# Kernel tuning notes

Hardware: AMD Instinct MI355X
Metric: run time of the kernel (lower is better)

## Reference

```python
import jax, jax.numpy as jnp
import numpy as np

N = 10000   # nodes
E = 160000  # edges (avg degree 16)
IN = 512
HID = 512
OUT = 512


def setup_inputs() -> dict:
    key = jax.random.key(0)
    ks = jax.random.split(key, 8)
    x = jax.random.normal(ks[0], (N, IN), dtype=jnp.float32)
    edge_index = jax.random.randint(ks[1], (2, E), 0, N, dtype=jnp.int64)
    def w(k, fi, fo):
        return jax.random.normal(k, (fi, fo), dtype=jnp.float32) * (1.0 / np.sqrt(fi)).astype(np.float32)
    return {
        "x": x,
        "edge_index": edge_index,
        "W1": w(ks[2], IN, HID), "b1": jnp.zeros((HID,), jnp.float32),
        "W2": w(ks[3], HID, HID), "b2": jnp.zeros((HID,), jnp.float32),
        "W3": w(ks[4], HID, OUT), "b3": jnp.zeros((OUT,), jnp.float32),
    }


def _gcn_norm(edge_index, n):
    # add self loops, then symmetric normalization D^{-1/2} (A+I) D^{-1/2}
    loops = jnp.arange(n, dtype=edge_index.dtype)
    row = jnp.concatenate([edge_index[0], loops])  # source
    col = jnp.concatenate([edge_index[1], loops])  # target (aggregation dim)
    deg = jax.ops.segment_sum(jnp.ones_like(col, jnp.float32), col, num_segments=n)
    dis = jnp.where(deg > 0, jax.lax.rsqrt(jnp.maximum(deg, 1.0)), 0.0)
    norm = dis[row] * dis[col]  # [E+N]
    return row, col, norm


def _gcn_layer(x, row, col, norm, W, b, n):
    h = x @ W                                    # [N, d_out] dense GEMM
    msg = h[row] * norm[:, None]                 # gather + scale, [E+N, d_out]
    out = jax.ops.segment_sum(msg, col, num_segments=n)  # scatter-add
    return out + b


def reference(x, edge_index, W1, b1, W2, b2, W3, b3):
    n = x.shape[0]
    row, col, norm = _gcn_norm(edge_index, n)
    h = _gcn_layer(x, row, col, norm, W1, b1, n)
    h = jax.nn.relu(h)  # dropout is identity in eval mode
    h = _gcn_layer(h, row, col, norm, W2, b2, n)
    h = jax.nn.relu(h)
    h = _gcn_layer(h, row, col, norm, W3, b3, n)
    return h
```

## Files before the change

kernel.cpp:

```cpp
#include <hip/hip_runtime.h>

typedef __attribute__((ext_vector_type(8))) short bf16x8;
typedef __attribute__((ext_vector_type(4))) float f32x4;

#define N_NODES 10000
#define N_EDGES 160000
#define FDIM    512
#define ELL     64
#define BM 64
#define BN 128
#define BK 64
#define TM 157
#define NGEMM (TM * 4)
#define NSCAT 625
#define NTRAN 768
#define NZERO 40
#define FBM 48
#define FNB 209
#define APAD 520

__device__ __forceinline__ float bf2f(unsigned int u) {
    union { unsigned int i; float f; } v; v.i = u << 16; return v.f;
}
__device__ __forceinline__ float bfs2f(short s) {
    return bf2f((unsigned int)(unsigned short)s);
}
__device__ __forceinline__ unsigned short f2bf(float f) {
    union { float f; unsigned int u; } v; v.f = f;
    unsigned int u = v.u;
    unsigned int r = u + 0x7fffu + ((u >> 16) & 1u);
    return (unsigned short)(r >> 16);
}
__device__ __forceinline__ void gload_lds16(const void* g, void* l) {
    __builtin_amdgcn_global_load_lds(
        (const __attribute__((address_space(1))) unsigned int*)g,
        (__attribute__((address_space(3))) unsigned int*)l, 16, 0, 0);
}
__device__ __forceinline__ int wave_is_f32(const unsigned int* w) {
    unsigned int v = w[(size_t)(threadIdx.x & 63) * 1000];
    unsigned int ex = (v >> 7) & 0xFFu;
    unsigned long long inb = __ballot(ex >= 100u && ex <= 140u);
    return (__popcll(inb) >= 48) ? 0 : 1;
}

__global__ __launch_bounds__(256) void prep_v8(
        const void* __restrict__ x, const void* __restrict__ ei,
        const void* __restrict__ W1, const void* __restrict__ W2,
        const void* __restrict__ W3, unsigned short* __restrict__ Wt,
        int* __restrict__ cnt, int* __restrict__ flags) {
    int b = blockIdx.x, tid = threadIdx.x;
    if (b < NTRAN) {
        __shared__ unsigned short tile[32][33];
        int z = b >> 8, t = b & 255;
        const void* W = (z == 0) ? W1 : (z == 1) ? W2 : W3;
        unsigned short* outp = Wt + (size_t)z * FDIM * FDIM;
        int ff32 = wave_is_f32((const unsigned int*)W);
        int tx = tid & 31, ty = tid >> 5;
        int xcol = (t & 15) * 32 + tx;
        int y0 = (t >> 4) * 32 + ty;
        #pragma unroll
        for (int j = 0; j < 32; j += 8) {
            int idx = (y0 + j) * FDIM + xcol;
            tile[ty + j][tx] = ff32 ? f2bf(((const float*)W)[idx])
                                    : ((const unsigned short*)W)[idx];
        }
        __syncthreads();
        int x2 = (t >> 4) * 32 + tx;
        int y2 = (t & 15) * 32 + ty;
        #pragma unroll
        for (int j = 0; j < 32; j += 8)
            outp[(y2 + j) * FDIM + x2] = tile[tx][ty + j];
    } else if (b < NTRAN + NZERO) {
        int i = (b - NTRAN) * 256 + tid;
        if (i < N_NODES) cnt[i] = 0;
    } else {
        if (tid < 64) {
            const unsigned long long* e64 = (const unsigned long long*)ei;
            unsigned long long v = e64[(size_t)tid * 2500];
            unsigned long long big = __ballot(v > 0xFFFFFFFFull);
            const unsigned int* xw = (const unsigned int*)x;
            unsigned int w = xw[(size_t)tid * 1000];
            unsigned int ex = (w >> 7) & 0xFFu;
            unsigned long long inb = __ballot(ex >= 100u && ex <= 140u);
            if (tid == 0) {
                flags[0] = (big == 0ull) ? 1 : 0;
                flags[1] = (__popcll(inb) >= 48) ? 0 : 1;
            }
        }
    }
}

__global__ __launch_bounds__(256) void gemm_scat_v8(
        const void* __restrict__ Ap, const unsigned short* __restrict__ Bt,
        unsigned short* __restrict__ C, const int* __restrict__ flags,
        const void* __restrict__ ei, int* __restrict__ cnt,
        int* __restrict__ ell) {
    __shared__ unsigned short As[BM * BK];
    __shared__ unsigned short Bs[BN * BK];
    if (blockIdx.x >= NGEMM) {
        int e = (blockIdx.x - NGEMM) * 256 + threadIdx.x;
        if (e < N_EDGES) {
            int r, c;
            if (flags[0]) {
                r = (int)((const long long*)ei)[e];
                c = (int)((const long long*)ei)[N_EDGES + e];
            } else {
                r = ((const int*)ei)[e];
                c = ((const int*)ei)[N_EDGES + e];
            }
            int slot = atomicAdd(&cnt[c], 1);
            if (slot < ELL) ell[(size_t)c * ELL + slot] = r;
        }
        return;
    }
    const int K = FDIM;
    const int af32 = flags[1];
    const int tid = threadIdx.x;
    const int t = blockIdx.x;
    const int bm = (t % TM) * BM, bn = (t / TM) * BN;
    const int lane = tid & 63, wv = tid >> 6;
    const int wm = (wv >> 1) * 32, wn = (wv & 1) * 64;
    const int lrow = lane & 15;
    const int tsl = lane >> 4;
    const int ksw = (lane & 7) ^ ((lane >> 3) & 7);
    const unsigned short* Abf = (const unsigned short*)Ap;
    f32x4 acc[2][4] = {};

    for (int k0 = 0; k0 < K; k0 += BK) {
        if (!af32) {
            #pragma unroll
            for (int j = 0; j < 2; ++j) {
                int r0 = wv * 16 + j * 8;
                int arow = bm + r0 + (lane >> 3);
                if (arow >= N_NODES) arow = N_NODES - 1;
                gload_lds16(Abf + (size_t)arow * K + k0 + ksw * 8, &As[r0 * BK]);
            }
            #pragma unroll
            for (int j = 0; j < 4; ++j) {
                int r0 = wv * 32 + j * 8;
                gload_lds16(Bt + (size_t)(bn + r0 + (lane >> 3)) * K + k0 + ksw * 8,
                            &Bs[r0 * BK]);
            }
        } else {
            #pragma unroll
            for (int j = 0; j < 4; ++j) {
                int r0 = wv * 32 + j * 8;
                gload_lds16(Bt + (size_t)(bn + r0 + (lane >> 3)) * K + k0 + ksw * 8,
                            &Bs[r0 * BK]);
            }
            #pragma unroll
            for (int i = 0; i < 2; ++i) {
                int c = tid + i * 256;
                int row = c >> 3, sl = c & 7;
                int grow = bm + row;
                bf16x8 va = {};
                if (grow < N_NODES) {
                    const float* Af = (const float*)Ap + (size_t)grow * K + k0 + sl * 8;
                    f32x4 lo = *(const f32x4*)Af;
                    f32x4 hi = *(const f32x4*)(Af + 4);
                    #pragma unroll
                    for (int jj = 0; jj < 4; ++jj) {
                        va[jj]     = (short)f2bf(lo[jj]);
                        va[4 + jj] = (short)f2bf(hi[jj]);
                    }
                }
                *(bf16x8*)(&As[row * BK + ((sl ^ (row & 7)) * 8)]) = va;
            }
        }
        __syncthreads();
        #pragma unroll
        for (int half = 0; half < 2; ++half) {
            int ts = half * 4 + tsl;
            bf16x8 af[2], bfr[4];
            #pragma unroll
            for (int f = 0; f < 2; ++f) {
                int row = wm + f * 16 + lrow;
                af[f] = *(const bf16x8*)(&As[row * BK + ((ts ^ (lrow & 7)) * 8)]);
            }
            #pragma unroll
            for (int f = 0; f < 4; ++f) {
                int row = wn + f * 16 + lrow;
                bfr[f] = *(const bf16x8*)(&Bs[row * BK + ((ts ^ (lrow & 7)) * 8)]);
            }
            #pragma unroll
            for (int fm = 0; fm < 2; ++fm)
                #pragma unroll
                for (int fn = 0; fn < 4; ++fn)
                    acc[fm][fn] = __builtin_amdgcn_mfma_f32_16x16x32_bf16(
                        af[fm], bfr[fn], acc[fm][fn], 0, 0, 0);
        }
        __syncthreads();
    }

    int crow = (lane >> 4) * 4;
    int ccol = lane & 15;
    #pragma unroll
    for (int fm = 0; fm < 2; ++fm)
        #pragma unroll
        for (int fn = 0; fn < 4; ++fn)
            #pragma unroll
            for (int r = 0; r < 4; ++r) {
                int row = bm + wm + fm * 16 + crow + r;
                if (row < N_NODES)
                    C[(size_t)row * FDIM + bn + wn + fn * 16 + ccol] =
                        f2bf(acc[fm][fn][r]);
            }
}

__global__ __launch_bounds__(384) void fused_ag_v8(
        const unsigned short* __restrict__ gin, const void* __restrict__ bias,
        const int* __restrict__ cnt, const int* __restrict__ ell,
        const unsigned short* __restrict__ Bt, unsigned short* __restrict__ Cout,
        const int* __restrict__ flags) {
    __shared__ unsigned short As[FBM * APAD];
    __shared__ unsigned short Bs[512 * 64];
    const int tid = threadIdx.x, lane = tid & 63, wv = tid / 64;
    const int bm = blockIdx.x * FBM;
    const int ff32 = flags[1];
    const int ksw = (lane & 7) ^ ((lane >> 3) & 7);

    for (int m = wv; m < 64; m += 6) {
        int r0 = m * 8;
        gload_lds16(Bt + (size_t)(r0 + (lane >> 3)) * FDIM + 0 + ksw * 8,
                    &Bs[r0 * 64]);
    }

    for (int rl = wv * 8; rl < wv * 8 + 8; ++rl) {
        int i = bm + rl;
        float a[8] = {};
        if (i < N_NODES) {
            int ci = cnt[i];
            int re = (ci > ELL) ? ELL : ci;
            const int* ep = ell + (size_t)i * ELL;
            int   srcl = (lane < re) ? ep[lane] : 0;
            int   cl   = (lane < re) ? cnt[srcl] : 0;
            float wl = rsqrtf((float)(cl + 1) * (float)(ci + 1));
            int j = 0;
            for (; j + 8 <= re; j += 8) {
                int s[8]; float w[8]; bf16x8 v[8];
                #pragma unroll
                for (int q = 0; q < 8; ++q) {
                    s[q] = __shfl(srcl, j + q); w[q] = __shfl(wl, j + q);
                }
                #pragma unroll
                for (int q = 0; q < 8; ++q)
                    v[q] = *(const bf16x8*)(gin + (size_t)s[q] * FDIM + lane * 8);
                #pragma unroll
                for (int q = 0; q < 8; ++q)
                    #pragma unroll
                    for (int tt = 0; tt < 8; ++tt) a[tt] += w[q] * bfs2f(v[q][tt]);
            }
            for (; j < re; ++j) {
                int s = __shfl(srcl, j); float w = __shfl(wl, j);
                bf16x8 v = *(const bf16x8*)(gin + (size_t)s * FDIM + lane * 8);
                #pragma unroll
                for (int tt = 0; tt < 8; ++tt) a[tt] += w * bfs2f(v[tt]);
            }
            float wself = 1.0f / (float)(ci + 1);
            bf16x8 vs = *(const bf16x8*)(gin + (size_t)i * FDIM + lane * 8);
            #pragma unroll
            for (int tt = 0; tt < 8; ++tt) a[tt] += wself * bfs2f(vs[tt]);
            if (ff32) {
                const float* B = (const float*)bias + lane * 8;
                #pragma unroll
                for (int tt = 0; tt < 8; ++tt) a[tt] += B[tt];
            } else {
                bf16x8 bb = *(const bf16x8*)((const unsigned short*)bias + lane * 8);
                #pragma unroll
                for (int tt = 0; tt < 8; ++tt) a[tt] += bfs2f(bb[tt]);
            }
            #pragma unroll
            for (int tt = 0; tt < 8; ++tt) a[tt] = fmaxf(a[tt], 0.f);
        }
        bf16x8 o;
        #pragma unroll
        for (int tt = 0; tt < 8; ++tt) o[tt] = (short)f2bf(a[tt]);
        *(bf16x8*)(&As[rl * APAD + lane * 8]) = o;
    }
    __syncthreads();

    const int wrow = wv % 3, wcol = wv / 3;
    const int lrow = lane & 15, tsl = lane >> 4;
    f32x4 acc[16] = {};
    for (int k0 = 0; k0 < FDIM; k0 += 64) {
        #pragma unroll
        for (int half = 0; half < 2; ++half) {
            bf16x8 af = *(const bf16x8*)(
                &As[(wrow * 16 + lrow) * APAD + k0 + half * 32 + tsl * 8]);
            int ts = half * 4 + tsl;
            #pragma unroll
            for (int ct = 0; ct < 16; ++ct) {
                int n = wcol * 256 + ct * 16 + lrow;
                bf16x8 bfr = *(const bf16x8*)(
                    &Bs[n * 64 + ((ts ^ (lrow & 7)) * 8)]);
                acc[ct] = __builtin_amdgcn_mfma_f32_16x16x32_bf16(
                    af, bfr, acc[ct], 0, 0, 0);
            }
        }
        __syncthreads();
        if (k0 + 64 < FDIM) {
            for (int m = wv; m < 64; m += 6) {
                int r0 = m * 8;
                gload_lds16(Bt + (size_t)(r0 + (lane >> 3)) * FDIM + (k0 + 64) + ksw * 8,
                            &Bs[r0 * 64]);
            }
        }
        __syncthreads();
    }
    int crow = (lane >> 4) * 4, ccol = lane & 15;
    #pragma unroll
    for (int ct = 0; ct < 16; ++ct)
        #pragma unroll
        for (int r = 0; r < 4; ++r) {
            int grow = bm + wrow * 16 + crow + r;
            if (grow < N_NODES)
                Cout[(size_t)grow * FDIM + wcol * 256 + ct * 16 + ccol] =
                    f2bf(acc[ct][r]);
        }
}

__global__ __launch_bounds__(256) void agg3_v8(
        const unsigned short* __restrict__ g, const void* __restrict__ bias,
        const int* __restrict__ cnt, const int* __restrict__ ell,
        void* __restrict__ out, const int* __restrict__ flags) {
    int wv = threadIdx.x >> 6, lane = threadIdx.x & 63;
    int i = blockIdx.x * 2 + (wv >> 1);
    int f = (wv & 1) * 256 + lane * 4;
    int ci = cnt[i];
    int re = (ci > ELL) ? ELL : ci;
    const int* ep = ell + (size_t)i * ELL;
    int   srcl = (lane < re) ? ep[lane] : 0;
    int   cl   = (lane < re) ? cnt[srcl] : 0;
    float wl = rsqrtf((float)(cl + 1) * (float)(ci + 1));
    float a0 = 0.f, a1 = 0.f, a2 = 0.f, a3 = 0.f;
    int j = 0;
    for (; j + 4 <= re; j += 4) {
        int s0 = __shfl(srcl, j);     float w0 = __shfl(wl, j);
        int s1 = __shfl(srcl, j + 1); float w1 = __shfl(wl, j + 1);
        int s2 = __shfl(srcl, j + 2); float w2 = __shfl(wl, j + 2);
        int s3 = __shfl(srcl, j + 3); float w3 = __shfl(wl, j + 3);
        uint2 v0 = *(const uint2*)(g + (size_t)s0 * FDIM + f);
        uint2 v1 = *(const uint2*)(g + (size_t)s1 * FDIM + f);
        uint2 v2 = *(const uint2*)(g + (size_t)s2 * FDIM + f);
        uint2 v3 = *(const uint2*)(g + (size_t)s3 * FDIM + f);
        a0 += w0 * bf2f(v0.x & 0xffffu); a1 += w0 * bf2f(v0.x >> 16);
        a2 += w0 * bf2f(v0.y & 0xffffu); a3 += w0 * bf2f(v0.y >> 16);
        a0 += w1 * bf2f(v1.x & 0xffffu); a1 += w1 * bf2f(v1.x >> 16);
        a2 += w1 * bf2f(v1.y & 0xffffu); a3 += w1 * bf2f(v1.y >> 16);
        a0 += w2 * bf2f(v2.x & 0xffffu); a1 += w2 * bf2f(v2.x >> 16);
        a2 += w2 * bf2f(v2.y & 0xffffu); a3 += w2 * bf2f(v2.y >> 16);
        a0 += w3 * bf2f(v3.x & 0xffffu); a1 += w3 * bf2f(v3.x >> 16);
        a2 += w3 * bf2f(v3.y & 0xffffu); a3 += w3 * bf2f(v3.y >> 16);
    }
    for (; j < re; ++j) {
        int s = __shfl(srcl, j); float w = __shfl(wl, j);
        uint2 v = *(const uint2*)(g + (size_t)s * FDIM + f);
        a0 += w * bf2f(v.x & 0xffffu); a1 += w * bf2f(v.x >> 16);
        a2 += w * bf2f(v.y & 0xffffu); a3 += w * bf2f(v.y >> 16);
    }
    float wself = 1.0f / (float)(ci + 1);
    uint2 vs = *(const uint2*)(g + (size_t)i * FDIM + f);
    a0 += wself * bf2f(vs.x & 0xffffu); a1 += wself * bf2f(vs.x >> 16);
    a2 += wself * bf2f(vs.y & 0xffffu); a3 += wself * bf2f(vs.y >> 16);
    int ff32 = flags[1];
    if (ff32) {
        f32x4 bb = *(const f32x4*)((const float*)bias + f);
        a0 += bb[0]; a1 += bb[1]; a2 += bb[2]; a3 += bb[3];
        f32x4 o = {a0, a1, a2, a3};
        *(f32x4*)((float*)out + (size_t)i * FDIM + f) = o;
    } else {
        uint2 bb = *(const uint2*)((const unsigned short*)bias + f);
        a0 += bf2f(bb.x & 0xffffu); a1 += bf2f(bb.x >> 16);
        a2 += bf2f(bb.y & 0xffffu); a3 += bf2f(bb.y >> 16);
        uint2 o;
        o.x = (unsigned int)f2bf(a0) | ((unsigned int)f2bf(a1) << 16);
        o.y = (unsigned int)f2bf(a2) | ((unsigned int)f2bf(a3) << 16);
        *(uint2*)((unsigned short*)out + (size_t)i * FDIM + f) = o;
    }
}

extern "C" void kernel_launch(void* const* d_in, const int* in_sizes, int n_in,
                              void* d_out, int out_size, void* d_ws, size_t ws_size,
                              hipStream_t stream) {
    (void)in_sizes; (void)n_in; (void)out_size; (void)ws_size;
    const void* x  = d_in[0];
    const void* ei = d_in[1];
    const void* W1 = d_in[2];
    const void* b1 = d_in[3];
    const void* W2 = d_in[4];
    const void* b2 = d_in[5];
    const void* W3 = d_in[6];
    const void* b3 = d_in[7];

    char* p = (char*)d_ws;
    auto alloc = [&](size_t bytes) -> void* {
        void* r = (void*)p;
        p += (bytes + 255) & ~(size_t)255;
        return r;
    };
    int*  flags = (int*) alloc(16);
    int*  cnt   = (int*) alloc((size_t)N_NODES * 4);
    int*  ell   = (int*) alloc((size_t)N_NODES * ELL * 4);
    unsigned short* Wt = (unsigned short*)alloc((size_t)3 * FDIM * FDIM * 2);
    unsigned short* g  = (unsigned short*)alloc((size_t)N_NODES * FDIM * 2);

    unsigned short* Wt1 = Wt;
    unsigned short* Wt2 = Wt + (size_t)FDIM * FDIM;
    unsigned short* Wt3 = Wt + (size_t)2 * FDIM * FDIM;
    unsigned short* h   = (unsigned short*)d_out;

    prep_v8<<<NTRAN + NZERO + 1, 256, 0, stream>>>(x, ei, W1, W2, W3, Wt, cnt, flags);
    gemm_scat_v8<<<NGEMM + NSCAT, 256, 0, stream>>>(x, Wt1, g, flags, ei, cnt, ell);
    fused_ag_v8<<<FNB, 384, 0, stream>>>(g, b1, cnt, ell, Wt2, h, flags);
    fused_ag_v8<<<FNB, 384, 0, stream>>>(h, b2, cnt, ell, Wt3, g, flags);
    agg3_v8<<<N_NODES / 2, 256, 0, stream>>>(g, b3, cnt, ell, d_out, flags);
}
```

Measured before the change: 228.6 us.

## Unfuse aggregation from GEMM and slice aggregation by feature columns

Replaces the fused aggregate-then-GEMM kernel, which used only 209 large blocks, with separate launches: a standalone GEMM per layer and a feature-sliced aggregation kernel. The aggregation splits the 512 features into 4 slices of 128 and launches one wave per node per slice, with 8-way unrolled gathers. The aim is more parallelism and better cache locality for the gathers, since each slice's working set is smaller. In exchange it adds extra kernel launches and an intermediate round trip through global memory for h.

```diff
diff --git a/kernel.cpp b/kernel.cpp
--- a/kernel.cpp
+++ b/kernel.cpp
@@ -15,15 +15,12 @@
 #define NSCAT 625
 #define NTRAN 768
 #define NZERO 40
-#define FBM 48
-#define FNB 209
-#define APAD 520
+#define SLICES 4
+#define SLW 128
+#define SLB 2500
 
 __device__ __forceinline__ float bf2f(unsigned int u) {
     union { unsigned int i; float f; } v; v.i = u << 16; return v.f;
-}
-__device__ __forceinline__ float bfs2f(short s) {
-    return bf2f((unsigned int)(unsigned short)s);
 }
 __device__ __forceinline__ unsigned short f2bf(float f) {
     union { float f; unsigned int u; } v; v.f = f;
@@ -43,7 +40,7 @@
     return (__popcll(inb) >= 48) ? 0 : 1;
 }
 
-__global__ __launch_bounds__(256) void prep_v8(
+__global__ __launch_bounds__(256) void prep_v9(
         const void* __restrict__ x, const void* __restrict__ ei,
         const void* __restrict__ W1, const void* __restrict__ W2,
         const void* __restrict__ W3, unsigned short* __restrict__ Wt,
@@ -90,11 +87,11 @@
     }
 }
 
-__global__ __launch_bounds__(256) void gemm_scat_v8(
+__global__ __launch_bounds__(256) void gemm_v9(
         const void* __restrict__ Ap, const unsigned short* __restrict__ Bt,
-        unsigned short* __restrict__ C, const int* __restrict__ flags,
-        const void* __restrict__ ei, int* __restrict__ cnt,
-        int* __restrict__ ell) {
+        unsigned short* __restrict__ C, int a_ext,
+        const int* __restrict__ flags, const void* __restrict__ ei,
+        int* __restrict__ cnt, int* __restrict__ ell) {
     __shared__ unsigned short As[BM * BK];
     __shared__ unsigned short Bs[BN * BK];
     if (blockIdx.x >= NGEMM) {
@@ -114,7 +111,7 @@
         return;
     }
     const int K = FDIM;
-    const int af32 = flags[1];
+    const int af32 = a_ext ? flags[1] : 0;
     const int tid = threadIdx.x;
     const int t = blockIdx.x;
     const int bm = (t % TM) * BM, bn = (t / TM) * BN;
@@ -207,175 +204,73 @@
             }
 }
 
-__global__ __launch_bounds__(384) void fused_ag_v8(
+__global__ __launch_bounds__(256) void agg_sl_v9(
         const unsigned short* __restrict__ gin, const void* __restrict__ bias,
         const int* __restrict__ cnt, const int* __restrict__ ell,
-        const unsigned short* __restrict__ Bt, unsigned short* __restrict__ Cout,
+        void* __restrict__ out, int relu, int out_ext,
         const int* __restrict__ flags) {
-    __shared__ unsigned short As[FBM * APAD];
-    __shared__ unsigned short Bs[512 * 64];
-    const int tid = threadIdx.x, lane = tid & 63, wv = tid / 64;
-    const int bm = blockIdx.x * FBM;
-    const int ff32 = flags[1];
-    const int ksw = (lane & 7) ^ ((lane >> 3) & 7);
-
-    for (int m = wv; m < 64; m += 6) {
-        int r0 = m * 8;
-        gload_lds16(Bt + (size_t)(r0 + (lane >> 3)) * FDIM + 0 + ksw * 8,
-                    &Bs[r0 * 64]);
-    }
-
-    for (int rl = wv * 8; rl < wv * 8 + 8; ++rl) {
-        int i = bm + rl;
-        float a[8] = {};
-        if (i < N_NODES) {
-            int ci = cnt[i];
-            int re = (ci > ELL) ? ELL : ci;
-            const int* ep = ell + (size_t)i * ELL;
-            int   srcl = (lane < re) ? ep[lane] : 0;
-            int   cl   = (lane < re) ? cnt[srcl] : 0;
-            float wl = rsqrtf((float)(cl + 1) * (float)(ci + 1));
-            int j = 0;
-            for (; j + 8 <= re; j += 8) {
-                int s[8]; float w[8]; bf16x8 v[8];
-                #pragma unroll
-                for (int q = 0; q < 8; ++q) {
-                    s[q] = __shfl(srcl, j + q); w[q] = __shfl(wl, j + q);
-                }
-                #pragma unroll
-                for (int q = 0; q < 8; ++q)
-                    v[q] = *(const bf16x8*)(gin + (size_t)s[q] * FDIM + lane * 8);
-                #pragma unroll
-                for (int q = 0; q < 8; ++q)
-                    #pragma unroll
-                    for (int tt = 0; tt < 8; ++tt) a[tt] += w[q] * bfs2f(v[q][tt]);
-            }
-            for (; j < re; ++j) {
-                int s = __shfl(srcl, j); float w = __shfl(wl, j);
-                bf16x8 v = *(const bf16x8*)(gin + (size_t)s * FDIM + lane * 8);
-                #pragma unroll
-                for (int tt = 0; tt < 8; ++tt) a[tt] += w * bfs2f(v[tt]);
-            }
-            float wself = 1.0f / (float)(ci + 1);
-            bf16x8 vs = *(const bf16x8*)(gin + (size_t)i * FDIM + lane * 8);
-            #pragma unroll
-            for (int tt = 0; tt < 8; ++tt) a[tt] += wself * bfs2f(vs[tt]);
-            if (ff32) {
-                const float* B = (const float*)bias + lane * 8;
-                #pragma unroll
-                for (int tt = 0; tt < 8; ++tt) a[tt] += B[tt];
-            } else {
-                bf16x8 bb = *(const bf16x8*)((const unsigned short*)bias + lane * 8);
-                #pragma unroll
-                for (int tt = 0; tt < 8; ++tt) a[tt] += bfs2f(bb[tt]);
-            }
-            #pragma unroll
-            for (int tt = 0; tt < 8; ++tt) a[tt] = fmaxf(a[tt], 0.f);
-        }
-        bf16x8 o;
-        #pragma unroll
-        for (int tt = 0; tt < 8; ++tt) o[tt] = (short)f2bf(a[tt]);
-        *(bf16x8*)(&As[rl * APAD + lane * 8]) = o;
-    }
-    __syncthreads();
-
-    const int wrow = wv % 3, wcol = wv / 3;
-    const int lrow = lane & 15, tsl = lane >> 4;
-    f32x4 acc[16] = {};
-    for (int k0 = 0; k0 < FDIM; k0 += 64) {
-        #pragma unroll
-        for (int half = 0; half < 2; ++half) {
-            bf16x8 af = *(const bf16x8*)(
-                &As[(wrow * 16 + lrow) * APAD + k0 + half * 32 + tsl * 8]);
-            int ts = half * 4 + tsl;
-            #pragma unroll
-            for (int ct = 0; ct < 16; ++ct) {
-                int n = wcol * 256 + ct * 16 + lrow;
-                bf16x8 bfr = *(const bf16x8*)(
-                    &Bs[n * 64 + ((ts ^ (lrow & 7)) * 8)]);
-                acc[ct] = __builtin_amdgcn_mfma_f32_16x16x32_bf16(
-                    af, bfr, acc[ct], 0, 0, 0);
-            }
-        }
-        __syncthreads();
-        if (k0 + 64 < FDIM) {
-            for (int m = wv; m < 64; m += 6) {
-                int r0 = m * 8;
-                gload_lds16(Bt + (size_t)(r0 + (lane >> 3)) * FDIM + (k0 + 64) + ksw * 8,
-                            &Bs[r0 * 64]);
-            }
-        }
-        __syncthreads();
-    }
-    int crow = (lane >> 4) * 4, ccol = lane & 15;
-    #pragma unroll
-    for (int ct = 0; ct < 16; ++ct)
-        #pragma unroll
-        for (int r = 0; r < 4; ++r) {
-            int grow = bm + wrow * 16 + crow + r;
-            if (grow < N_NODES)
-                Cout[(size_t)grow * FDIM + wcol * 256 + ct * 16 + ccol] =
-                    f2bf(acc[ct][r]);
-        }
-}
-
-__global__ __launch_bounds__(256) void agg3_v8(
-        const unsigned short* __restrict__ g, const void* __restrict__ bias,
-        const int* __restrict__ cnt, const int* __restrict__ ell,
-        void* __restrict__ out, const int* __restrict__ flags) {
-    int wv = threadIdx.x >> 6, lane = threadIdx.x & 63;
-    int i = blockIdx.x * 2 + (wv >> 1);
-    int f = (wv & 1) * 256 + lane * 4;
+    const int wv = threadIdx.x >> 6, lane = threadIdx.x & 63;
+    const int slice = blockIdx.x / SLB;
+    const int i = (blockIdx.x % SLB) * 4 + wv;
+    const int fu = slice * (SLW / 2) + lane;
+    const unsigned int* g32 = (const unsigned int*)gin;
     int ci = cnt[i];
     int re = (ci > ELL) ? ELL : ci;
     const int* ep = ell + (size_t)i * ELL;
     int   srcl = (lane < re) ? ep[lane] : 0;
     int   cl   = (lane < re) ? cnt[srcl] : 0;
-    float wl = rsqrtf((float)(cl + 1) * (float)(ci + 1));
-    float a0 = 0.f, a1 = 0.f, a2 = 0.f, a3 = 0.f;
+    float wl   = rsqrtf((float)(cl + 1) * (float)(ci + 1));
+    float a0 = 0.f, a1 = 0.f;
     int j = 0;
-    for (; j + 4 <= re; j += 4) {
+    for (; j + 8 <= re; j += 8) {
         int s0 = __shfl(srcl, j);     float w0 = __shfl(wl, j);
         int s1 = __shfl(srcl, j + 1); float w1 = __shfl(wl, j + 1);
         int s2 = __shfl(srcl, j + 2); float w2 = __shfl(wl, j + 2);
         int s3 = __shfl(srcl, j + 3); float w3 = __shfl(wl, j + 3);
-        uint2 v0 = *(const uint2*)(g + (size_t)s0 * FDIM + f);
-        uint2 v1 = *(const uint2*)(g + (size_t)s1 * FDIM + f);
-        uint2 v2 = *(const uint2*)(g + (size_t)s2 * FDIM + f);
-        uint2 v3 = *(const uint2*)(g + (size_t)s3 * FDIM + f);
-        a0 += w0 * bf2f(v0.x & 0xffffu); a1 += w0 * bf2f(v0.x >> 16);
-        a2 += w0 * bf2f(v0.y & 0xffffu); a3 += w0 * bf2f(v0.y >> 16);
-        a0 += w1 * bf2f(v1.x & 0xffffu); a1 += w1 * bf2f(v1.x >> 16);
-        a2 += w1 * bf2f(v1.y & 0xffffu); a3 += w1 * bf2f(v1.y >> 16);
-        a0 += w2 * bf2f(v2.x & 0xffffu); a1 += w2 * bf2f(v2.x >> 16);
-        a2 += w2 * bf2f(v2.y & 0xffffu); a3 += w2 * bf2f(v2.y >> 16);
-        a0 += w3 * bf2f(v3.x & 0xffffu); a1 += w3 * bf2f(v3.x >> 16);
-        a2 += w3 * bf2f(v3.y & 0xffffu); a3 += w3 * bf2f(v3.y >> 16);
+        int s4 = __shfl(srcl, j + 4); float w4 = __shfl(wl, j + 4);
+        int s5 = __shfl(srcl, j + 5); float w5 = __shfl(wl, j + 5);
+        int s6 = __shfl(srcl, j + 6); float w6 = __shfl(wl, j + 6);
+        int s7 = __shfl(srcl, j + 7); float w7 = __shfl(wl, j + 7);
+        unsigned int v0 = g32[(size_t)s0 * 256 + fu];
+        unsigned int v1 = g32[(size_t)s1 * 256 + fu];
+        unsigned int v2 = g32[(size_t)s2 * 256 + fu];
+        unsigned int v3 = g32[(size_t)s3 * 256 + fu];
+        unsigned int v4 = g32[(size_t)s4 * 256 + fu];
+        unsigned int v5 = g32[(size_t)s5 * 256 + fu];
+        unsigned int v6 = g32[(size_t)s6 * 256 + fu];
+        unsigned int v7 = g32[(size_t)s7 * 256 + fu];
+        a0 += w0 * bf2f(v0 & 0xffffu); a1 += w0 * bf2f(v0 >> 16);
+        a0 += w1 * bf2f(v1 & 0xffffu); a1 += w1 * bf2f(v1 >> 16);
+        a0 += w2 * bf2f(v2 & 0xffffu); a1 += w2 * bf2f(v2 >> 16);
+        a0 += w3 * bf2f(v3 & 0xffffu); a1 += w3 * bf2f(v3 >> 16);
+        a0 += w4 * bf2f(v4 & 0xffffu); a1 += w4 * bf2f(v4 >> 16);
+        a0 += w5 * bf2f(v5 & 0xffffu); a1 += w5 * bf2f(v5 >> 16);
+        a0 += w6 * bf2f(v6 & 0xffffu); a1 += w6 * bf2f(v6 >> 16);
+        a0 += w7 * bf2f(v7 & 0xffffu); a1 += w7 * bf2f(v7 >> 16);
     }
     for (; j < re; ++j) {
         int s = __shfl(srcl, j); float w = __shfl(wl, j);
-        uint2 v = *(const uint2*)(g + (size_t)s * FDIM + f);
-        a0 += w * bf2f(v.x & 0xffffu); a1 += w * bf2f(v.x >> 16);
-        a2 += w * bf2f(v.y & 0xffffu); a3 += w * bf2f(v.y >> 16);
+        unsigned int v = g32[(size_t)s * 256 + fu];
+        a0 += w * bf2f(v & 0xffffu); a1 += w * bf2f(v >> 16);
     }
     float wself = 1.0f / (float)(ci + 1);
-    uint2 vs = *(const uint2*)(g + (size_t)i * FDIM + f);
-    a0 += wself * bf2f(vs.x & 0xffffu); a1 += wself * bf2f(vs.x >> 16);
-    a2 += wself * bf2f(vs.y & 0xffffu); a3 += wself * bf2f(vs.y >> 16);
+    unsigned int vs = g32[(size_t)i * 256 + fu];
+    a0 += wself * bf2f(vs & 0xffffu); a1 += wself * bf2f(vs >> 16);
     int ff32 = flags[1];
     if (ff32) {
-        f32x4 bb = *(const f32x4*)((const float*)bias + f);
-        a0 += bb[0]; a1 += bb[1]; a2 += bb[2]; a3 += bb[3];
-        f32x4 o = {a0, a1, a2, a3};
-        *(f32x4*)((float*)out + (size_t)i * FDIM + f) = o;
+        const float* B = (const float*)bias + fu * 2;
+        a0 += B[0]; a1 += B[1];
     } else {
-        uint2 bb = *(const uint2*)((const unsigned short*)bias + f);
-        a0 += bf2f(bb.x & 0xffffu); a1 += bf2f(bb.x >> 16);
-        a2 += bf2f(bb.y & 0xffffu); a3 += bf2f(bb.y >> 16);
-        uint2 o;
-        o.x = (unsigned int)f2bf(a0) | ((unsigned int)f2bf(a1) << 16);
-        o.y = (unsigned int)f2bf(a2) | ((unsigned int)f2bf(a3) << 16);
-        *(uint2*)((unsigned short*)out + (size_t)i * FDIM + f) = o;
+        unsigned int bb = ((const unsigned int*)bias)[fu];
+        a0 += bf2f(bb & 0xffffu); a1 += bf2f(bb >> 16);
+    }
+    if (relu) { a0 = fmaxf(a0, 0.f); a1 = fmaxf(a1, 0.f); }
+    if (out_ext && ff32) {
+        float2 o = {a0, a1};
+        *(float2*)((float*)out + (size_t)i * FDIM + fu * 2) = o;
+    } else {
+        unsigned int o = (unsigned int)f2bf(a0) | ((unsigned int)f2bf(a1) << 16);
+        ((unsigned int*)out)[(size_t)i * 256 + fu] = o;
     }
 }
 
@@ -409,9 +304,11 @@
     unsigned short* Wt3 = Wt + (size_t)2 * FDIM * FDIM;
     unsigned short* h   = (unsigned short*)d_out;
 
-    prep_v8<<<NTRAN + NZERO + 1, 256, 0, stream>>>(x, ei, W1, W2, W3, Wt, cnt, flags);
-    gemm_scat_v8<<<NGEMM + NSCAT, 256, 0, stream>>>(x, Wt1, g, flags, ei, cnt, ell);
-    fused_ag_v8<<<FNB, 384, 0, stream>>>(g, b1, cnt, ell, Wt2, h, flags);
-    fused_ag_v8<<<FNB, 384, 0, stream>>>(h, b2, cnt, ell, Wt3, g, flags);
-    agg3_v8<<<N_NODES / 2, 256, 0, stream>>>(g, b3, cnt, ell, d_out, flags);
-}
+    prep_v9<<<NTRAN + NZERO + 1, 256, 0, stream>>>(x, ei, W1, W2, W3, Wt, cnt, flags);
+    gemm_v9<<<NGEMM + NSCAT, 256, 0, stream>>>(x, Wt1, g, 1, flags, ei, cnt, ell);
+    agg_sl_v9<<<SLICES * SLB, 256, 0, stream>>>(g, b1, cnt, ell, h, 1, 0, flags);
+    gemm_v9<<<NGEMM, 256, 0, stream>>>(h, Wt2, g, 0, flags, ei, cnt, ell);
+    agg_sl_v9<<<SLICES * SLB, 256, 0, stream>>>(g, b2, cnt, ell, h, 1, 0, flags);
+    gemm_v9<<<NGEMM, 256, 0, stream>>>(h, Wt3, g, 0, flags, ei, cnt, ell);
+    agg_sl_v9<<<SLICES * SLB, 256, 0, stream>>>(g, b3, cnt, ell, d_out, 0, 1, flags);
+}
```

Result: faster. 207.7 us (-9.1%).
